# Kernel tuning notes

Measured on AMD Instinct MI355X. Metric: run time of the kernel, lower is better.

Reference implementation:

```python
import jax, jax.numpy as jnp
import numpy as np

B, T, E, H, DEPTH = 128, 256, 512, 1024, 3


def setup_inputs() -> dict:
    key = jax.random.key(0)
    ks = jax.random.split(key, 9)
    s_e = 1.0 / np.sqrt(E)
    s_h = 1.0 / np.sqrt(H)
    return {
        "x": jax.random.normal(ks[0], (B, T, E), jnp.float32),
        "W_ih0": jax.random.normal(ks[1], (4 * H, E), jnp.float32) * s_e,
        "W_hh0": jax.random.normal(ks[2], (4 * H, H), jnp.float32) * s_h,
        "b_ih0": jax.random.normal(ks[3], (4 * H,), jnp.float32) * s_h,
        "b_hh0": jax.random.normal(ks[4], (4 * H,), jnp.float32) * s_h,
        "W_ih_r": jax.random.normal(ks[5], (DEPTH - 1, 4 * H, H), jnp.float32) * s_h,
        "W_hh_r": jax.random.normal(ks[6], (DEPTH - 1, 4 * H, H), jnp.float32) * s_h,
        "b_ih_r": jax.random.normal(ks[7], (DEPTH - 1, 4 * H), jnp.float32) * s_h,
        "b_hh_r": jax.random.normal(ks[8], (DEPTH - 1, 4 * H), jnp.float32) * s_h,
        "trainable": 1,
    }


def _lstm_cell(inp, h, c, Wih, Whh, bih, bhh):
    # torch.nn.LSTMCell: gates = inp @ Wih.T + bih + h @ Whh.T + bhh; order i,f,g,o
    gates = inp @ Wih.T + bih + h @ Whh.T + bhh
    i, f, g, o = jnp.split(gates, 4, axis=-1)
    c_new = jax.nn.sigmoid(f) * c + jax.nn.sigmoid(i) * jnp.tanh(g)
    h_new = jax.nn.sigmoid(o) * jnp.tanh(c_new)
    return h_new, c_new


def reference(x, W_ih0, W_hh0, b_ih0, b_hh0, W_ih_r, W_hh_r, b_ih_r, b_hh_r, trainable):
    b, _, _ = x.shape
    h_dim = W_hh0.shape[1]
    n_rest = W_ih_r.shape[0]
    zeros = jnp.zeros((b, h_dim), x.dtype)
    x_t = jnp.swapaxes(x, 0, 1)  # [T, B, E]

    def step(carry, xt):
        hs, cs = carry  # each [n_rest, B, H]
        # faithful bug: layer-0 state is never updated -> always zeros
        h, c = _lstm_cell(xt, zeros, zeros, W_ih0, W_hh0, b_ih0, b_hh0)
        new_h, new_c = [], []
        for l in range(n_rest):  # small fixed depth loop
            h, c = _lstm_cell(h, hs[l], cs[l], W_ih_r[l], W_hh_r[l], b_ih_r[l], b_hh_r[l])
            new_h.append(h)
            new_c.append(c)
        return (jnp.stack(new_h), jnp.stack(new_c)), h

    init = (jnp.zeros((n_rest, b, h_dim), x.dtype),
            jnp.zeros((n_rest, b, h_dim), x.dtype))
    _, out = jax.lax.scan(step, init, x_t)
    return out  # [T, B, H] == list of top-layer h per timestep
```

## Files before the change

### kernel.cpp

```cpp
#include <hip/hip_runtime.h>

static constexpr int Bc = 128;
static constexpr int Tc = 256;
static constexpr int Ec = 512;
static constexpr int Hc = 1024;
static constexpr int SLOT = Bc * Hc;

using bf16x8 = __attribute__((ext_vector_type(8))) short;
using f32x4  = __attribute__((ext_vector_type(4))) float;

__device__ __forceinline__ unsigned short f2bf(float f) {
  unsigned int u = __float_as_uint(f);
  u += 0x7FFFu + ((u >> 16) & 1u);
  return (unsigned short)(u >> 16);
}
__device__ __forceinline__ float sigm(float x) { return 1.0f / (1.0f + __expf(-x)); }
__device__ __forceinline__ float ftanh(float x) { return 1.0f - 2.0f / (__expf(2.0f * x) + 1.0f); }

#define MFMA16(A, Bf, C) __builtin_amdgcn_mfma_f32_16x16x32_bf16((A), (Bf), (C), 0, 0, 0)

__device__ __forceinline__ void poll_rlx(const int* p, int tgt) {
  while (__hip_atomic_load(p, __ATOMIC_RELAXED, __HIP_MEMORY_SCOPE_AGENT) < tgt)
    __builtin_amdgcn_s_sleep(1);
}
__device__ __forceinline__ void sig(int* p, int v) {
  __hip_atomic_store(p, v, __ATOMIC_RELAXED, __HIP_MEMORY_SCOPE_AGENT);
}
__device__ __forceinline__ void stg_c(unsigned short* p, unsigned short v) {
  __hip_atomic_store(p, v, __ATOMIC_RELAXED, __HIP_MEMORY_SCOPE_AGENT);
}
__device__ __forceinline__ int lds_acq(const int* p) {
  return __hip_atomic_load(p, __ATOMIC_ACQUIRE, __HIP_MEMORY_SCOPE_WORKGROUP);
}
__device__ __forceinline__ void lds_rel(int* p, int v) {
  __hip_atomic_store(p, v, __ATOMIC_RELEASE, __HIP_MEMORY_SCOPE_WORKGROUP);
}

__global__ void k_cvt_bf16(const float* __restrict__ src, unsigned short* __restrict__ dst, int n) {
  int i = (blockIdx.x * blockDim.x + threadIdx.x) * 4;
  if (i + 3 < n) {
    f32x4 v = *(const f32x4*)(src + i);
    *(ushort4*)(dst + i) = make_ushort4(f2bf(v[0]), f2bf(v[1]), f2bf(v[2]), f2bf(v[3]));
  }
}

__global__ void k_prep_small(const float* __restrict__ bih0, const float* __restrict__ bhh0,
                             float* __restrict__ b0s,
                             unsigned short* __restrict__ h2c,
                             int* __restrict__ f1, int* __restrict__ f2) {
  int i = blockIdx.x * blockDim.x + threadIdx.x;
  if (i < 4096) b0s[i] = bih0[i] + bhh0[i];
  h2c[i] = 0;
  if (i < 128 * 16) { f1[i] = 0; f2[i] = 0; }
}

__global__ __launch_bounds__(512, 1) void k_l0(
    const unsigned short* __restrict__ xb, const unsigned short* __restrict__ W0,
    const float* __restrict__ b0s, unsigned short* __restrict__ H0)
{
  const int tid = threadIdx.x;
  const int lane = tid & 63, wid = tid >> 6;
  const int wM = wid >> 2, wN = wid & 3;
  const int rowbase = blockIdx.x * 32 + wM * 16;
  const int jbase   = blockIdx.y * 64 + wN * 16;
  const int ri = lane & 15, kg = lane >> 4;

  const int r = rowbase + ri;
  const int t = r >> 7, b = r & (Bc - 1);
  const unsigned short* arow = xb + ((size_t)b * Tc + t) * Ec + kg * 8;

  const unsigned short* w0r = W0 + ((size_t)(0 * Hc + jbase + ri)) * Ec + kg * 8;
  const unsigned short* w2r = W0 + ((size_t)(2 * Hc + jbase + ri)) * Ec + kg * 8;
  const unsigned short* w3r = W0 + ((size_t)(3 * Hc + jbase + ri)) * Ec + kg * 8;

  f32x4 ai = {0,0,0,0}, ag = {0,0,0,0}, ao = {0,0,0,0};
#pragma unroll
  for (int kk = 0; kk < Ec / 32; ++kk) {
    bf16x8 a = *(const bf16x8*)(arow + kk * 32);
    ai = MFMA16(a, *(const bf16x8*)(w0r + kk * 32), ai);
    ag = MFMA16(a, *(const bf16x8*)(w2r + kk * 32), ag);
    ao = MFMA16(a, *(const bf16x8*)(w3r + kk * 32), ao);
  }
  const int j = jbase + ri;
  const float bi = b0s[j], bg = b0s[2 * Hc + j], bo = b0s[3 * Hc + j];
#pragma unroll
  for (int q = 0; q < 4; ++q) {
    const int rr = rowbase + kg * 4 + q;
    float c = sigm(ai[q] + bi) * ftanh(ag[q] + bg);
    float h = sigm(ao[q] + bo) * ftanh(c);
    H0[(size_t)(rr >> 7) * SLOT + (size_t)(j >> 3) * 1024 + (size_t)(rr & 127) * 8 + (j & 7)] = f2bf(h);
  }
}

__global__ __launch_bounds__(512, 1) void k_rec(
    const unsigned short* H0,
    const float* __restrict__ Wih, const float* __restrict__ Whh,
    const float* __restrict__ bih, const float* __restrict__ bhh,
    unsigned short* h1c,
    unsigned short* h2c,
    int* f1, int* f2,
    float* out)
{
  __shared__ unsigned short Wlds[2 * 64 * 64 * 8];
  __shared__ float pbuf[4][4][64][4];
  __shared__ int flg[32];
  int* sF_   = flg + 0;
  int* sG_   = flg + 4;
  int* pollD = flg + 8;
  int* pollF = flg + 12;
  int* doneS = flg + 16;

  const int tid = threadIdx.x;
  const int lane = tid & 63, wid = tid >> 6;
  const int m = wid & 3;
  const bool gatedw = (wid >= 4);
  const int bid = blockIdx.x;
  const int layer = bid >> 7;
  const int w = bid & 127;
  const int j0 = w * 8;
  const int ri = lane & 15, kg = lane >> 4;

  if (tid < 32) flg[tid] = 0;

  const size_t lw = (size_t)layer * 4096 * 1024;
  for (int s = tid; s < 2 * 64 * 64; s += 512) {
    const int l   = s & 63;
    const int kkg = (s >> 6) & 63;
    const int t   = s >> 12;
    const int rr  = l & 15;
    const int gate = t * 2 + (rr >> 3);
    const int R = gate * 1024 + j0 + (rr & 7);
    const int k = kkg * 32 + (l >> 4) * 8;
    const float* src = (k < 1024) ? (Wih + lw + (size_t)R * 1024 + k)
                                  : (Whh + lw + (size_t)R * 1024 + (k - 1024));
    f32x4 v0 = *(const f32x4*)src;
    f32x4 v1 = *(const f32x4*)(src + 4);
    ushort4* d = (ushort4*)(Wlds + (size_t)s * 8);
    d[0] = make_ushort4(f2bf(v0[0]), f2bf(v0[1]), f2bf(v0[2]), f2bf(v0[3]));
    d[1] = make_ushort4(f2bf(v1[0]), f2bf(v1[1]), f2bf(v1[2]), f2bf(v1[3]));
  }

  const int jme = j0 + (ri & 7);
  const int g0 = (ri < 8) ? 0 : 1;
  const int g1 = (ri < 8) ? 2 : 3;
  const float bias0 = bih[layer * 4096 + g0 * 1024 + jme] + bhh[layer * 4096 + g0 * 1024 + jme];
  const float bias1 = bih[layer * 4096 + g1 * 1024 + jme] + bhh[layer * 4096 + g1 * 1024 + jme];

  float c0[4]  = {0.f, 0.f, 0.f, 0.f};
  float c1s[4] = {0.f, 0.f, 0.f, 0.f};

  const unsigned short* lds0 = Wlds + (size_t)lane * 8;
  const unsigned short* lds1 = Wlds + (size_t)64 * 64 * 8 + (size_t)lane * 8;
  const int abase = kg * 1024 + (m * 32 + ri) * 8;
  const bool lo = (ri < 8);

  f32x4 acc00, acc01, acc10, acc11;
#define ZERO4() { acc00 = (f32x4){0,0,0,0}; acc01 = (f32x4){0,0,0,0}; \
                  acc10 = (f32x4){0,0,0,0}; acc11 = (f32x4){0,0,0,0}; }
#define PLOAD()  { acc00 = *(const f32x4*)&pbuf[m][0][lane][0]; \
                   acc01 = *(const f32x4*)&pbuf[m][1][lane][0]; \
                   acc10 = *(const f32x4*)&pbuf[m][2][lane][0]; \
                   acc11 = *(const f32x4*)&pbuf[m][3][lane][0]; }
#define PWRITE() { *(f32x4*)&pbuf[m][0][lane][0] = acc00; \
                   *(f32x4*)&pbuf[m][1][lane][0] = acc01; \
                   *(f32x4*)&pbuf[m][2][lane][0] = acc10; \
                   *(f32x4*)&pbuf[m][3][lane][0] = acc11; }

#define HALF_MM4(Abase, LDSOFF)                                             \
  {                                                                         \
    const unsigned short* ap_ = (Abase) + abase;                            \
    _Pragma("unroll")                                                       \
    for (int kk = 0; kk < 32; ++kk) {                                       \
      bf16x8 b0 = *(const bf16x8*)(lds0 + (LDSOFF) + kk * 512);             \
      bf16x8 b1 = *(const bf16x8*)(lds1 + (LDSOFF) + kk * 512);             \
      bf16x8 vlo = *(const bf16x8*)(ap_ + kk * 4096);                       \
      bf16x8 vhi = *(const bf16x8*)(ap_ + kk * 4096 + 128);                 \
      acc00 = MFMA16(vlo, b0, acc00);                                       \
      acc01 = MFMA16(vlo, b1, acc01);                                       \
      acc10 = MFMA16(vhi, b0, acc10);                                       \
      acc11 = MFMA16(vhi, b1, acc11);                                       \
    }                                                                       \
  }

#define CELL4(accA, accB, cre, hnarr)                                       \
  _Pragma("unroll")                                                         \
  for (int q = 0; q < 4; ++q) {                                             \
    float x0 = accA[q] + bias0;                                             \
    float x1 = accB[q] + bias1;                                             \
    float p0 = __shfl_xor(x0, 8);                                           \
    float p1 = __shfl_xor(x1, 8);                                           \
    float gi = lo ? x0 : p0;                                                \
    float gf = lo ? p0 : x0;                                                \
    float gg = lo ? x1 : p1;                                                \
    float go = lo ? p1 : x1;                                                \
    float cn = sigm(gf) * cre[q] + sigm(gi) * ftanh(gg);                    \
    hnarr[q] = sigm(go) * ftanh(cn);                                        \
    cre[q] = cn;                                                            \
  }

#define GPOLL_BAR(farr, tgt, stamp)                                         \
  { if (lane < 32) poll_rlx((farr) + (m * 32 + lane) * 16, (tgt));          \
    if (lane == 0) lds_rel(&(stamp)[m], (tgt));                             \
    while (lds_acq(&(stamp)[0]) < (tgt) || lds_acq(&(stamp)[1]) < (tgt) ||  \
           lds_acq(&(stamp)[2]) < (tgt) || lds_acq(&(stamp)[3]) < (tgt)) {} }

  __syncthreads();

  if (layer == 0) {
    if (!gatedw) {
      ZERO4() HALF_MM4(H0, 0)
      for (int t = 0; t < Tc; ++t) {
        while (lds_acq(&sG_[m]) < t) {}
        PWRITE()
        if (lane == 0) lds_rel(&sF_[m], t + 1);
        if (t + 1 < Tc) { ZERO4() HALF_MM4(H0 + (size_t)(t + 1) * SLOT, 0) }
      }
    } else {
      for (int p = 0; p < Tc; ++p) {
        if (p >= 1) GPOLL_BAR(f1, p, pollD)
        while (lds_acq(&sF_[m]) < p + 1) {}
        PLOAD()
        if (lane == 0) lds_rel(&sG_[m], p + 1);
        if (p >= 1) HALF_MM4(h1c + (size_t)(p - 1) * SLOT, 32 * 512)
        float hn0[4], hn1[4];
        CELL4(acc00, acc01, c0, hn0)
        CELL4(acc10, acc11, c1s, hn1)
        if (lo) {
          unsigned short* hb = h1c + (size_t)p * SLOT + (size_t)w * 1024 + (ri & 7);
#pragma unroll
          for (int q = 0; q < 4; ++q) {
            const int r0 = m * 32 + kg * 4 + q;
            stg_c(hb + (size_t)r0 * 8, f2bf(hn0[q]));
            stg_c(hb + (size_t)(r0 + 16) * 8, f2bf(hn1[q]));
          }
        }
        __asm__ volatile("s_waitcnt vmcnt(0)" ::: "memory");
        if (lane == 0) lds_rel(&doneS[m], p + 1);
        if (m == 0) {
          while (lds_acq(&doneS[1]) < p + 1 || lds_acq(&doneS[2]) < p + 1 ||
                 lds_acq(&doneS[3]) < p + 1) {}
          if (lane == 0) sig(f1 + w * 16, p + 1);
        }
      }
    }
  } else {
    if (!gatedw) {
      GPOLL_BAR(f1, 1, pollF)
      ZERO4() HALF_MM4(h1c, 0)
      for (int t = 0; t < Tc; ++t) {
        while (lds_acq(&sG_[m]) < t) {}
        PWRITE()
        if (lane == 0) lds_rel(&sF_[m], t + 1);
        if (t + 1 < Tc) {
          GPOLL_BAR(f1, t + 2, pollF)
          ZERO4() HALF_MM4(h1c + (size_t)(t + 1) * SLOT, 0)
        }
      }
    } else {
      for (int s = 0; s < Tc; ++s) {
        if (s >= 1) GPOLL_BAR(f2, s, pollD)
        __builtin_amdgcn_fence(__ATOMIC_ACQUIRE, "agent");
        while (lds_acq(&sF_[m]) < s + 1) {}
        PLOAD()
        if (lane == 0) lds_rel(&sG_[m], s + 1);
        HALF_MM4(h2c + (size_t)((s - 1) & 3) * SLOT, 32 * 512)
        float hn0[4], hn1[4];
        CELL4(acc00, acc01, c0, hn0)
        CELL4(acc10, acc11, c1s, hn1)
        if (lo) {
          unsigned short* hb = h2c + (size_t)(s & 3) * SLOT + (size_t)w * 1024 + (ri & 7);
#pragma unroll
          for (int q = 0; q < 4; ++q) {
            const int r0 = m * 32 + kg * 4 + q;
            stg_c(hb + (size_t)r0 * 8, f2bf(hn0[q]));
            stg_c(hb + (size_t)(r0 + 16) * 8, f2bf(hn1[q]));
          }
        }
        __asm__ volatile("s_waitcnt vmcnt(0)" ::: "memory");
        if (lane == 0) lds_rel(&doneS[m], s + 1);
        if (m == 0) {
          while (lds_acq(&doneS[1]) < s + 1 || lds_acq(&doneS[2]) < s + 1 ||
                 lds_acq(&doneS[3]) < s + 1) {}
          if (lane == 0) sig(f2 + w * 16, s + 1);
        }
        if (lo) {
          float* po = out + (size_t)s * SLOT;
#pragma unroll
          for (int q = 0; q < 4; ++q) {
            const int r0 = m * 32 + kg * 4 + q;
            po[(size_t)r0 * Hc + jme] = hn0[q];
            po[(size_t)(r0 + 16) * Hc + jme] = hn1[q];
          }
        }
      }
    }
  }
}

extern "C" void kernel_launch(void* const* d_in, const int* in_sizes, int n_in,
                              void* d_out, int out_size, void* d_ws, size_t ws_size,
                              hipStream_t stream) {
  const float* x     = (const float*)d_in[0];
  const float* W_ih0 = (const float*)d_in[1];
  const float* b_ih0 = (const float*)d_in[3];
  const float* b_hh0 = (const float*)d_in[4];
  const float* W_ihr = (const float*)d_in[5];
  const float* W_hhr = (const float*)d_in[6];
  const float* b_ihr = (const float*)d_in[7];
  const float* b_hhr = (const float*)d_in[8];

  char* ws = (char*)d_ws;
  constexpr size_t H0_OFF  = 0;
  constexpr size_t H2B_OFF = H0_OFF + (size_t)Tc * SLOT * 2;
  constexpr size_t F1_OFF  = H2B_OFF + (size_t)4 * SLOT * 2;
  constexpr size_t F2_OFF  = F1_OFF + 128 * 16 * 4;

  unsigned short* H0  = (unsigned short*)(ws + H0_OFF);
  unsigned short* h2c = (unsigned short*)(ws + H2B_OFF);
  float* b0s = (float*)(ws + F2_OFF + 128 * 16 * 4);
  int* f1 = (int*)(ws + F1_OFF);
  int* f2 = (int*)(ws + F2_OFF);

  unsigned short* xb  = (unsigned short*)d_out;
  unsigned short* W0b = (unsigned short*)d_out + (size_t)Bc * Tc * Ec;
  unsigned short* h1c = (unsigned short*)d_out + (size_t)Tc * SLOT;
  float* out = (float*)d_out;

  int n0 = 4096 * 512;
  k_cvt_bf16<<<n0 / 1024, 256, 0, stream>>>(W_ih0, W0b, n0);
  int nx = Bc * Tc * Ec;
  k_cvt_bf16<<<nx / 1024, 256, 0, stream>>>(x, xb, nx);
  k_prep_small<<<2048, 256, 0, stream>>>(b_ih0, b_hh0, b0s, h2c, f1, f2);
  k_l0<<<dim3(1024, 16), 512, 0, stream>>>(xb, W0b, b0s, H0);

  k_rec<<<dim3(256), dim3(512), 0, stream>>>(H0, W_ihr, W_hhr, b_ihr, b_hhr,
                                             h1c, h2c, f1, f2, out);
}
```

Before: 4.720 ms.

## Split recurrent-step poll barrier into halves and overlap with MMA

The gated recurrent loops no longer wait for all four wave-groups' flags before starting the h@Whh product. The K loop is split in two, and each half starts as soon as the flags covering its K range are seen. Flag polling drops the s_sleep backoff, and layer 2 replaces the agent-scope acquire fence with relaxed atomic 8-byte loads of h. This is meant to cut serialization latency on the per-timestep critical path. In exchange it adds busy-spinning pressure and relies on relaxed atomic loads for visibility.

```diff
diff --git a/kernel.cpp b/kernel.cpp
--- a/kernel.cpp
+++ b/kernel.cpp
@@ -23,11 +23,20 @@
   while (__hip_atomic_load(p, __ATOMIC_RELAXED, __HIP_MEMORY_SCOPE_AGENT) < tgt)
     __builtin_amdgcn_s_sleep(1);
 }
+__device__ __forceinline__ void poll_fast(const int* p, int tgt) {
+  while (__hip_atomic_load(p, __ATOMIC_RELAXED, __HIP_MEMORY_SCOPE_AGENT) < tgt) {}
+}
 __device__ __forceinline__ void sig(int* p, int v) {
   __hip_atomic_store(p, v, __ATOMIC_RELAXED, __HIP_MEMORY_SCOPE_AGENT);
 }
 __device__ __forceinline__ void stg_c(unsigned short* p, unsigned short v) {
   __hip_atomic_store(p, v, __ATOMIC_RELAXED, __HIP_MEMORY_SCOPE_AGENT);
+}
+__device__ __forceinline__ bf16x8 ldg_c(const unsigned short* p) {
+  union { unsigned long long u[2]; bf16x8 v; } r;
+  r.u[0] = __hip_atomic_load((const unsigned long long*)p,       __ATOMIC_RELAXED, __HIP_MEMORY_SCOPE_AGENT);
+  r.u[1] = __hip_atomic_load((const unsigned long long*)(p + 4), __ATOMIC_RELAXED, __HIP_MEMORY_SCOPE_AGENT);
+  return r.v;
 }
 __device__ __forceinline__ int lds_acq(const int* p) {
   return __hip_atomic_load(p, __ATOMIC_ACQUIRE, __HIP_MEMORY_SCOPE_WORKGROUP);
@@ -166,15 +175,31 @@
                    *(f32x4*)&pbuf[m][2][lane][0] = acc10; \
                    *(f32x4*)&pbuf[m][3][lane][0] = acc11; }
 
-#define HALF_MM4(Abase, LDSOFF)                                             \
+#define HALF_MM4R(Abase, LDSOFF, K0, K1)                                    \
   {                                                                         \
     const unsigned short* ap_ = (Abase) + abase;                            \
     _Pragma("unroll")                                                       \
-    for (int kk = 0; kk < 32; ++kk) {                                       \
+    for (int kk = (K0); kk < (K1); ++kk) {                                  \
       bf16x8 b0 = *(const bf16x8*)(lds0 + (LDSOFF) + kk * 512);             \
       bf16x8 b1 = *(const bf16x8*)(lds1 + (LDSOFF) + kk * 512);             \
       bf16x8 vlo = *(const bf16x8*)(ap_ + kk * 4096);                       \
       bf16x8 vhi = *(const bf16x8*)(ap_ + kk * 4096 + 128);                 \
+      acc00 = MFMA16(vlo, b0, acc00);                                       \
+      acc01 = MFMA16(vlo, b1, acc01);                                       \
+      acc10 = MFMA16(vhi, b0, acc10);                                       \
+      acc11 = MFMA16(vhi, b1, acc11);                                       \
+    }                                                                       \
+  }
+
+#define HALF_MM4C(Abase, LDSOFF, K0, K1)                                    \
+  {                                                                         \
+    const unsigned short* ap_ = (Abase) + abase;                            \
+    _Pragma("unroll")                                                       \
+    for (int kk = (K0); kk < (K1); ++kk) {                                  \
+      bf16x8 b0 = *(const bf16x8*)(lds0 + (LDSOFF) + kk * 512);             \
+      bf16x8 b1 = *(const bf16x8*)(lds1 + (LDSOFF) + kk * 512);             \
+      bf16x8 vlo = ldg_c(ap_ + kk * 4096);                                  \
+      bf16x8 vhi = ldg_c(ap_ + kk * 4096 + 128);                            \
       acc00 = MFMA16(vlo, b0, acc00);                                       \
       acc01 = MFMA16(vlo, b1, acc01);                                       \
       acc10 = MFMA16(vhi, b0, acc10);                                       \
@@ -208,20 +233,29 @@
 
   if (layer == 0) {
     if (!gatedw) {
-      ZERO4() HALF_MM4(H0, 0)
+      ZERO4() HALF_MM4R(H0, 0, 0, 32)
       for (int t = 0; t < Tc; ++t) {
         while (lds_acq(&sG_[m]) < t) {}
         PWRITE()
         if (lane == 0) lds_rel(&sF_[m], t + 1);
-        if (t + 1 < Tc) { ZERO4() HALF_MM4(H0 + (size_t)(t + 1) * SLOT, 0) }
+        if (t + 1 < Tc) { ZERO4() HALF_MM4R(H0 + (size_t)(t + 1) * SLOT, 0, 0, 32) }
       }
     } else {
       for (int p = 0; p < Tc; ++p) {
-        if (p >= 1) GPOLL_BAR(f1, p, pollD)
+        if (p >= 1) {
+          if (lane < 32) poll_fast(f1 + (m * 32 + lane) * 16, p);
+          if (lane == 0) lds_rel(&pollD[m], p);
+        }
         while (lds_acq(&sF_[m]) < p + 1) {}
         PLOAD()
         if (lane == 0) lds_rel(&sG_[m], p + 1);
-        if (p >= 1) HALF_MM4(h1c + (size_t)(p - 1) * SLOT, 32 * 512)
+        if (p >= 1) {
+          const unsigned short* gb = h1c + (size_t)(p - 1) * SLOT;
+          while (lds_acq(&pollD[0]) < p || lds_acq(&pollD[1]) < p) {}
+          HALF_MM4R(gb, 32 * 512, 0, 16)
+          while (lds_acq(&pollD[2]) < p || lds_acq(&pollD[3]) < p) {}
+          HALF_MM4R(gb, 32 * 512, 16, 32)
+        }
         float hn0[4], hn1[4];
         CELL4(acc00, acc01, c0, hn0)
         CELL4(acc10, acc11, c1s, hn1)
@@ -246,24 +280,32 @@
   } else {
     if (!gatedw) {
       GPOLL_BAR(f1, 1, pollF)
-      ZERO4() HALF_MM4(h1c, 0)
+      ZERO4() HALF_MM4R(h1c, 0, 0, 32)
       for (int t = 0; t < Tc; ++t) {
         while (lds_acq(&sG_[m]) < t) {}
         PWRITE()
         if (lane == 0) lds_rel(&sF_[m], t + 1);
         if (t + 1 < Tc) {
           GPOLL_BAR(f1, t + 2, pollF)
-          ZERO4() HALF_MM4(h1c + (size_t)(t + 1) * SLOT, 0)
+          ZERO4() HALF_MM4R(h1c + (size_t)(t + 1) * SLOT, 0, 0, 32)
         }
       }
     } else {
       for (int s = 0; s < Tc; ++s) {
-        if (s >= 1) GPOLL_BAR(f2, s, pollD)
-        __builtin_amdgcn_fence(__ATOMIC_ACQUIRE, "agent");
+        if (s >= 1) {
+          if (lane < 32) poll_fast(f2 + (m * 32 + lane) * 16, s);
+          if (lane == 0) lds_rel(&pollD[m], s);
+        }
         while (lds_acq(&sF_[m]) < s + 1) {}
         PLOAD()
         if (lane == 0) lds_rel(&sG_[m], s + 1);
-        HALF_MM4(h2c + (size_t)((s - 1) & 3) * SLOT, 32 * 512)
+        {
+          const unsigned short* gb = h2c + (size_t)((s - 1) & 3) * SLOT;
+          if (s >= 1) { while (lds_acq(&pollD[0]) < s || lds_acq(&pollD[1]) < s) {} }
+          HALF_MM4C(gb, 32 * 512, 0, 16)
+          if (s >= 1) { while (lds_acq(&pollD[2]) < s || lds_acq(&pollD[3]) < s) {} }
+          HALF_MM4C(gb, 32 * 512, 16, 32)
+        }
         float hn0[4], hn1[4];
         CELL4(acc00, acc01, c0, hn0)
         CELL4(acc10, acc11, c1s, hn1)
```

Result: slower. 4.876 ms (+3.3%).

## Retile layer-0 GEMM to stage a timestep's x block in swizzled LDS

Applied to the files above, without the earlier changes.

The layer-0 input-projection kernel now gives each block one timestep's full 128x512 activation tile, loaded once into LDS with an XOR swizzle. Each of the 4 waves keeps 8 row-tiles of accumulators, so every weight fragment loaded from global memory is reused across 8 MFMAs instead of 1. This cuts redundant global reads of both x and W0, at the cost of much higher register pressure (96 accumulator floats per lane) and 128KB of LDS per block. It only affects the layer-0 precompute; the recurrent kernel, which probably dominates the runtime, is unchanged.

```diff
diff --git a/kernel.cpp b/kernel.cpp
--- a/kernel.cpp
+++ b/kernel.cpp
@@ -54,41 +54,62 @@
   if (i < 128 * 16) { f1[i] = 0; f2[i] = 0; }
 }
 
-__global__ __launch_bounds__(512, 1) void k_l0(
+__global__ __launch_bounds__(256, 1) void k_l0(
     const unsigned short* __restrict__ xb, const unsigned short* __restrict__ W0,
     const float* __restrict__ b0s, unsigned short* __restrict__ H0)
 {
+  __shared__ unsigned short Axs[64 * 128 * 8];
   const int tid = threadIdx.x;
   const int lane = tid & 63, wid = tid >> 6;
-  const int wM = wid >> 2, wN = wid & 3;
-  const int rowbase = blockIdx.x * 32 + wM * 16;
-  const int jbase   = blockIdx.y * 64 + wN * 16;
+  const int bx = blockIdx.x;
+  const int jbase = blockIdx.y * 64 + wid * 16;
   const int ri = lane & 15, kg = lane >> 4;
 
-  const int r = rowbase + ri;
-  const int t = r >> 7, b = r & (Bc - 1);
-  const unsigned short* arow = xb + ((size_t)b * Tc + t) * Ec + kg * 8;
-
-  const unsigned short* w0r = W0 + ((size_t)(0 * Hc + jbase + ri)) * Ec + kg * 8;
-  const unsigned short* w2r = W0 + ((size_t)(2 * Hc + jbase + ri)) * Ec + kg * 8;
-  const unsigned short* w3r = W0 + ((size_t)(3 * Hc + jbase + ri)) * Ec + kg * 8;
-
-  f32x4 ai = {0,0,0,0}, ag = {0,0,0,0}, ao = {0,0,0,0};
-#pragma unroll
-  for (int kk = 0; kk < Ec / 32; ++kk) {
-    bf16x8 a = *(const bf16x8*)(arow + kk * 32);
-    ai = MFMA16(a, *(const bf16x8*)(w0r + kk * 32), ai);
-    ag = MFMA16(a, *(const bf16x8*)(w2r + kk * 32), ag);
-    ao = MFMA16(a, *(const bf16x8*)(w3r + kk * 32), ao);
-  }
+  for (int i = tid; i < 8192; i += 256) {
+    const int row = i >> 6;
+    const int chunk = i & 63;
+    const int phys = chunk * 128 + (row ^ (chunk & 15));
+    *(bf16x8*)(Axs + (size_t)phys * 8) =
+        *(const bf16x8*)(xb + ((size_t)row * Tc + bx) * Ec + chunk * 8);
+  }
+  __syncthreads();
+
   const int j = jbase + ri;
   const float bi = b0s[j], bg = b0s[2 * Hc + j], bo = b0s[3 * Hc + j];
-#pragma unroll
-  for (int q = 0; q < 4; ++q) {
-    const int rr = rowbase + kg * 4 + q;
-    float c = sigm(ai[q] + bi) * ftanh(ag[q] + bg);
-    float h = sigm(ao[q] + bo) * ftanh(c);
-    H0[(size_t)(rr >> 7) * SLOT + (size_t)(j >> 3) * 1024 + (size_t)(rr & 127) * 8 + (j & 7)] = f2bf(h);
+  const unsigned short* w0r = W0 + ((size_t)(0 * Hc + j)) * Ec + kg * 8;
+  const unsigned short* w2r = W0 + ((size_t)(2 * Hc + j)) * Ec + kg * 8;
+  const unsigned short* w3r = W0 + ((size_t)(3 * Hc + j)) * Ec + kg * 8;
+
+  f32x4 ai[8], ag[8], ao[8];
+#pragma unroll
+  for (int u = 0; u < 8; ++u) { ai[u] = (f32x4){0,0,0,0}; ag[u] = (f32x4){0,0,0,0}; ao[u] = (f32x4){0,0,0,0}; }
+
+#pragma unroll 4
+  for (int kk = 0; kk < Ec / 32; ++kk) {
+    bf16x8 wi = *(const bf16x8*)(w0r + kk * 32);
+    bf16x8 wg = *(const bf16x8*)(w2r + kk * 32);
+    bf16x8 wo = *(const bf16x8*)(w3r + kk * 32);
+    const int ch = kk * 4 + kg;
+#pragma unroll
+    for (int u = 0; u < 8; ++u) {
+      const int phys = ch * 128 + ((u * 16 + ri) ^ (ch & 15));
+      bf16x8 a = *(const bf16x8*)(Axs + (size_t)phys * 8);
+      ai[u] = MFMA16(a, wi, ai[u]);
+      ag[u] = MFMA16(a, wg, ag[u]);
+      ao[u] = MFMA16(a, wo, ao[u]);
+    }
+  }
+
+  unsigned short* hb = H0 + (size_t)bx * SLOT + (size_t)(j >> 3) * 1024 + (j & 7);
+#pragma unroll
+  for (int u = 0; u < 8; ++u) {
+#pragma unroll
+    for (int q = 0; q < 4; ++q) {
+      const int b = u * 16 + kg * 4 + q;
+      float c = sigm(ai[u][q] + bi) * ftanh(ag[u][q] + bg);
+      float h = sigm(ao[u][q] + bo) * ftanh(c);
+      hb[(size_t)b * 8] = f2bf(h);
+    }
   }
 }
 
@@ -331,7 +352,7 @@
   int nx = Bc * Tc * Ec;
   k_cvt_bf16<<<nx / 1024, 256, 0, stream>>>(x, xb, nx);
   k_prep_small<<<2048, 256, 0, stream>>>(b_ih0, b_hh0, b0s, h2c, f1, f2);
-  k_l0<<<dim3(1024, 16), 512, 0, stream>>>(xb, W0b, b0s, H0);
+  k_l0<<<dim3(Tc, 16), 256, 0, stream>>>(xb, W0b, b0s, H0);
 
   k_rec<<<dim3(256), dim3(512), 0, stream>>>(H0, W_ihr, W_hhr, b_ihr, b_hhr,
                                              h1c, h2c, f1, f2, out);
```

Result: faster. 4.143 ms (-12.2%).
